# Kernel tuning notes

Measured on AMD Instinct MI355X. Metric: run time of the kernel, lower is better.

## Reference

```python
import jax, jax.numpy as jnp
import numpy as np

N_NODES = 100000
N_EDGES = 3200000
IN_SIZE = 256
HID_SIZE = 256
OUT_SIZE = 64


def setup_inputs() -> dict:
    key = jax.random.key(0)
    ks = jax.random.split(key, 8)
    X = jax.random.normal(ks[0], (N_NODES, IN_SIZE), dtype=jnp.float32)
    edge_vals = jax.random.uniform(ks[1], (N_EDGES,), dtype=jnp.float32)
    # xavier-uniform-ish init for weights
    lim1 = float(np.sqrt(6.0 / (IN_SIZE + HID_SIZE)))
    W1 = jax.random.uniform(ks[2], (IN_SIZE, HID_SIZE), minval=-lim1, maxval=lim1, dtype=jnp.float32)
    b1 = jnp.zeros((HID_SIZE,), dtype=jnp.float32)
    lim2 = float(np.sqrt(6.0 / (HID_SIZE + OUT_SIZE)))
    W2 = jax.random.uniform(ks[3], (HID_SIZE, OUT_SIZE), minval=-lim2, maxval=lim2, dtype=jnp.float32)
    b2 = jnp.zeros((OUT_SIZE,), dtype=jnp.float32)
    row = jnp.sort(jax.random.randint(ks[4], (N_EDGES,), 0, N_NODES, dtype=jnp.int32))
    col = jax.random.randint(ks[5], (N_EDGES,), 0, N_NODES, dtype=jnp.int32)
    return {"X": X, "edge_vals": edge_vals, "W1": W1, "b1": b1,
            "W2": W2, "b2": b2, "row": row, "col": col}


def reference(X, edge_vals, W1, b1, W2, b2, row, col):
    """2-layer GCN (eval mode, dropout = identity).

    A is a sparse NxN matrix in COO form: A[row[e], col[e]] = edge_vals[e].
    Layer: relu(A @ (X @ W1) + b1); output: A @ (h @ W2) + b2.
    """
    n = X.shape[0]

    def spmm(dense):  # (A @ dense): gather columns, scale, segment-sum over rows
        gathered = edge_vals[:, None] * dense[col]        # [E, F]
        return jax.ops.segment_sum(gathered, row, num_segments=n)

    h = spmm(X @ W1) + b1          # [N, HID]
    h = jax.nn.relu(h)
    out = spmm(h @ W2) + b2        # [N, OUT]
    return out
```

## Files before the change

### kernel.cpp

```cpp
#include <hip/hip_runtime.h>


constexpr int IN_SIZE = 256;
constexpr int HID = 256;
constexpr int OUTF = 64;

typedef __bf16 bf16x8 __attribute__((ext_vector_type(8)));
typedef float f32x4 __attribute__((ext_vector_type(4)));

__device__ __forceinline__ ushort f2b(float f) {
    uint u = __float_as_uint(f);
    uint r = (u + 0x7fffu + ((u >> 16) & 1u)) >> 16;
    return (ushort)r;
}
__device__ __forceinline__ float b2f(ushort h) {
    return __uint_as_float(((uint)h) << 16);
}

__global__ void setup_kernel(const int* __restrict__ row, int* __restrict__ rp,
                             const float* __restrict__ W1, ushort* __restrict__ W1T,
                             const float* __restrict__ W2, ushort* __restrict__ W2T,
                             int n, int E, int rpB) {
    int b = blockIdx.x;
    if (b < rpB) {
        int i = b * 256 + threadIdx.x;
        if (i > n) return;
        int lo = 0, hi = E;
        while (lo < hi) {
            int mid = (lo + hi) >> 1;
            if (row[mid] < i) lo = mid + 1; else hi = mid;
        }
        rp[i] = lo;
    } else if (b < rpB + 256) {
        int nn = b - rpB;
        int k = threadIdx.x;
        W1T[(size_t)nn * 256 + k] = f2b(W1[(size_t)k * 256 + nn]);
    } else {
        int nn = b - rpB - 256;
        int k = threadIdx.x;
        W2T[(size_t)nn * 256 + k] = f2b(W2[(size_t)k * 64 + nn]);
    }
}

__global__ void prep_edges(const float* __restrict__ vals, const int* __restrict__ col,
                           const float* __restrict__ s, int2* __restrict__ ew,
                           int E, int shift) {
    int e = blockIdx.x * 256 + threadIdx.x;
    if (e >= E) return;
    int c = col[e];
    ew[e] = make_int2(c << shift, __float_as_int(vals[e] * s[c]));
}

__global__ __launch_bounds__(512)
void gemm1_q(const float* __restrict__ A, const ushort* __restrict__ Bt,
             char* __restrict__ Q, float* __restrict__ s1, int M) {
    constexpr int K = 256;
    __shared__ ushort As[128 * 40];
    __shared__ ushort Bs[256 * 40];
    __shared__ float red[4][128];
    __shared__ float fin[128];
    const int tid = threadIdx.x;
    const int wave = tid >> 6, lane = tid & 63;
    const int quad = lane >> 4, l = lane & 15;
    const int wr = wave >> 2, wc = wave & 3;
    const int m0 = blockIdx.x * 128;

    const int ar = tid >> 2;
    const int ak = (tid & 3) * 8;
    const size_t aoff = (size_t)min(m0 + ar, M - 1) * K + ak;
    const int bn = tid >> 2;
    const int bkp = (tid & 3) * 8;

    f32x4 acc[4][4] = {};

    for (int k0 = 0; k0 < K; k0 += 32) {
        float4 a0 = *(const float4*)(A + aoff + k0);
        float4 a1 = *(const float4*)(A + aoff + k0 + 4);
        uint4 bv0 = *(const uint4*)(Bt + (size_t)bn * K + k0 + bkp);
        uint4 bv1 = *(const uint4*)(Bt + (size_t)(bn + 128) * K + k0 + bkp);
        uint4 pa;
        pa.x = (uint)f2b(a0.x) | ((uint)f2b(a0.y) << 16);
        pa.y = (uint)f2b(a0.z) | ((uint)f2b(a0.w) << 16);
        pa.z = (uint)f2b(a1.x) | ((uint)f2b(a1.y) << 16);
        pa.w = (uint)f2b(a1.z) | ((uint)f2b(a1.w) << 16);
        __syncthreads();
        *(uint4*)&As[ar * 40 + ak] = pa;
        *(uint4*)&Bs[bn * 40 + bkp] = bv0;
        *(uint4*)&Bs[(bn + 128) * 40 + bkp] = bv1;
        __syncthreads();

        bf16x8 af[4], bfr[4];
#pragma unroll
        for (int mt = 0; mt < 4; ++mt)
            af[mt] = *(const bf16x8*)&As[(wr * 64 + mt * 16 + l) * 40 + quad * 8];
#pragma unroll
        for (int nt = 0; nt < 4; ++nt)
            bfr[nt] = *(const bf16x8*)&Bs[(wc * 64 + nt * 16 + l) * 40 + quad * 8];
#pragma unroll
        for (int mt = 0; mt < 4; ++mt)
#pragma unroll
            for (int nt = 0; nt < 4; ++nt)
                acc[mt][nt] = __builtin_amdgcn_mfma_f32_16x16x32_bf16(
                    af[mt], bfr[nt], acc[mt][nt], 0, 0, 0);
    }

    float rmax[4][4];
#pragma unroll
    for (int mt = 0; mt < 4; ++mt)
#pragma unroll
        for (int reg = 0; reg < 4; ++reg) {
            float m = 0.f;
#pragma unroll
            for (int nt = 0; nt < 4; ++nt)
                m = fmaxf(m, fabsf(acc[mt][nt][reg]));
            rmax[mt][reg] = m;
        }
#pragma unroll
    for (int s = 1; s <= 8; s <<= 1)
#pragma unroll
        for (int mt = 0; mt < 4; ++mt)
#pragma unroll
            for (int reg = 0; reg < 4; ++reg)
                rmax[mt][reg] = fmaxf(rmax[mt][reg], __shfl_xor(rmax[mt][reg], s));
    if (l < 4) {
#pragma unroll
        for (int mt = 0; mt < 4; ++mt)
            red[wc][wr * 64 + mt * 16 + quad * 4 + l] = rmax[mt][l];
    }
    __syncthreads();
    if (tid < 128) {
        float m = fmaxf(fmaxf(red[0][tid], red[1][tid]),
                        fmaxf(red[2][tid], red[3][tid]));
        fin[tid] = m;
        int r = m0 + tid;
        if (r < M) s1[r] = m * (1.f / 127.f);
    }
    __syncthreads();

#pragma unroll
    for (int mt = 0; mt < 4; ++mt)
#pragma unroll
        for (int reg = 0; reg < 4; ++reg) {
            int rl = wr * 64 + mt * 16 + quad * 4 + reg;
            int r = m0 + rl;
            if (r >= M) continue;
            float m = fin[rl];
            float inv = m > 0.f ? 127.f / m : 0.f;
#pragma unroll
            for (int nt = 0; nt < 4; ++nt) {
                int c = wc * 64 + nt * 16 + l;
                Q[(size_t)r * 256 + c] = (char)(int)rintf(acc[mt][nt][reg] * inv);
            }
        }
}

__global__ __launch_bounds__(256, 4)
void gemm2_q(const ushort* __restrict__ A, const ushort* __restrict__ Bt,
             char* __restrict__ Q, float* __restrict__ s2, int M) {
    constexpr int K = 256;
    __shared__ ushort As[128 * 40];
    __shared__ ushort Bs[64 * 40];
    __shared__ float red[2][128];
    __shared__ float fin[128];
    const int tid = threadIdx.x;
    const int wave = tid >> 6, lane = tid & 63;
    const int quad = lane >> 4, l = lane & 15;
    const int wr = wave >> 1, wc = wave & 1;
    const int m0 = blockIdx.x * 128;

    const int crow = tid >> 2;
    const int cpart = (tid & 3) * 8;
    const size_t aoff0 = (size_t)min(m0 + crow, M - 1) * K + cpart;
    const size_t aoff1 = (size_t)min(m0 + crow + 64, M - 1) * K + cpart;
    const size_t boff  = (size_t)crow * K + cpart;

    f32x4 acc[4][2] = {};

    for (int k0 = 0; k0 < K; k0 += 32) {
        uint4 a0 = *(const uint4*)(A + aoff0 + k0);
        uint4 a1 = *(const uint4*)(A + aoff1 + k0);
        uint4 b0 = *(const uint4*)(Bt + boff + k0);
        __syncthreads();
        *(uint4*)&As[crow * 40 + cpart] = a0;
        *(uint4*)&As[(crow + 64) * 40 + cpart] = a1;
        *(uint4*)&Bs[crow * 40 + cpart] = b0;
        __syncthreads();

        bf16x8 af[4], bfr[2];
        const ushort* ab = &As[(wr * 64 + l) * 40 + quad * 8];
#pragma unroll
        for (int mt = 0; mt < 4; ++mt)
            af[mt] = *(const bf16x8*)(ab + mt * 16 * 40);
        const ushort* bb = &Bs[(wc * 32 + l) * 40 + quad * 8];
#pragma unroll
        for (int nt = 0; nt < 2; ++nt)
            bfr[nt] = *(const bf16x8*)(bb + nt * 16 * 40);
#pragma unroll
        for (int mt = 0; mt < 4; ++mt)
#pragma unroll
            for (int nt = 0; nt < 2; ++nt)
                acc[mt][nt] = __builtin_amdgcn_mfma_f32_16x16x32_bf16(
                    af[mt], bfr[nt], acc[mt][nt], 0, 0, 0);
    }

    float rmax[4][4];
#pragma unroll
    for (int mt = 0; mt < 4; ++mt)
#pragma unroll
        for (int reg = 0; reg < 4; ++reg)
            rmax[mt][reg] = fmaxf(fabsf(acc[mt][0][reg]), fabsf(acc[mt][1][reg]));
#pragma unroll
    for (int s = 1; s <= 8; s <<= 1)
#pragma unroll
        for (int mt = 0; mt < 4; ++mt)
#pragma unroll
            for (int reg = 0; reg < 4; ++reg)
                rmax[mt][reg] = fmaxf(rmax[mt][reg], __shfl_xor(rmax[mt][reg], s));
    if (l < 4) {
#pragma unroll
        for (int mt = 0; mt < 4; ++mt)
            red[wc][wr * 64 + mt * 16 + quad * 4 + l] = rmax[mt][l];
    }
    __syncthreads();
    if (tid < 128) {
        float m = fmaxf(red[0][tid], red[1][tid]);
        fin[tid] = m;
        int r = m0 + tid;
        if (r < M) s2[r] = m * (1.f / 127.f);
    }
    __syncthreads();

#pragma unroll
    for (int mt = 0; mt < 4; ++mt)
#pragma unroll
        for (int reg = 0; reg < 4; ++reg) {
            int rl = wr * 64 + mt * 16 + quad * 4 + reg;
            int r = m0 + rl;
            if (r >= M) continue;
            float m = fin[rl];
            float inv = m > 0.f ? 127.f / m : 0.f;
#pragma unroll
            for (int nt = 0; nt < 2; ++nt) {
                int c = wc * 32 + nt * 16 + l;
                Q[(size_t)r * 64 + c] = (char)(int)rintf(acc[mt][nt][reg] * inv);
            }
        }
}

__global__ __launch_bounds__(256)
void spmm1_q(const char* __restrict__ Q, const int2* __restrict__ ew,
             const int* __restrict__ rp, const float* __restrict__ bias,
             ushort* __restrict__ H, int n) {
    const int wave = threadIdx.x >> 6;
    const int lane = threadIdx.x & 63;
    const int node = blockIdx.x * 4 + wave;
    if (node >= n) return;
    const int e0 = rp[node], e1 = rp[node + 1];
    float a0 = 0.f, a1 = 0.f, a2 = 0.f, a3 = 0.f;
    int e = e0;
    for (; e + 7 < e1; e += 8) {
#pragma unroll
        for (int u = 0; u < 8; ++u) {
            int2 m = ew[e + u];
            float w = __int_as_float(m.y);
            char4 q = *(const char4*)(Q + (size_t)(uint)m.x + lane * 4);
            a0 += w * (float)q.x;
            a1 += w * (float)q.y;
            a2 += w * (float)q.z;
            a3 += w * (float)q.w;
        }
    }
    for (; e < e1; ++e) {
        int2 m = ew[e];
        float w = __int_as_float(m.y);
        char4 q = *(const char4*)(Q + (size_t)(uint)m.x + lane * 4);
        a0 += w * (float)q.x;
        a1 += w * (float)q.y;
        a2 += w * (float)q.z;
        a3 += w * (float)q.w;
    }
    float4 b = *(const float4*)(bias + lane * 4);
    ushort4 r;
    r.x = f2b(fmaxf(a0 + b.x, 0.f));
    r.y = f2b(fmaxf(a1 + b.y, 0.f));
    r.z = f2b(fmaxf(a2 + b.z, 0.f));
    r.w = f2b(fmaxf(a3 + b.w, 0.f));
    *(ushort4*)(H + (size_t)node * 256 + lane * 4) = r;
}

__global__ __launch_bounds__(256)
void spmm2_q(const char* __restrict__ Q, const int2* __restrict__ ew,
             const int* __restrict__ rp, const float* __restrict__ bias,
             float* __restrict__ O, int n) {
    const int wave = threadIdx.x >> 6;
    const int lane = threadIdx.x & 63;
    const int node = blockIdx.x * 4 + wave;
    if (node >= n) return;
    const int e0 = rp[node], e1 = rp[node + 1];
    float acc = 0.f;
    int e = e0;
    for (; e + 15 < e1; e += 16) {
#pragma unroll
        for (int u = 0; u < 16; ++u) {
            int2 m = ew[e + u];
            acc += __int_as_float(m.y) * (float)Q[(size_t)(uint)m.x + lane];
        }
    }
    for (; e + 3 < e1; e += 4) {
#pragma unroll
        for (int u = 0; u < 4; ++u) {
            int2 m = ew[e + u];
            acc += __int_as_float(m.y) * (float)Q[(size_t)(uint)m.x + lane];
        }
    }
    for (; e < e1; ++e) {
        int2 m = ew[e];
        acc += __int_as_float(m.y) * (float)Q[(size_t)(uint)m.x + lane];
    }
    O[(size_t)node * 64 + lane] = acc + bias[lane];
}

static inline size_t alignup(size_t x) { return (x + 255) & ~(size_t)255; }

extern "C" void kernel_launch(void* const* d_in, const int* in_sizes, int n_in,
                              void* d_out, int out_size, void* d_ws, size_t ws_size,
                              hipStream_t stream) {
    const float* X  = (const float*)d_in[0];
    const float* ev = (const float*)d_in[1];
    const float* W1 = (const float*)d_in[2];
    const float* b1 = (const float*)d_in[3];
    const float* W2 = (const float*)d_in[4];
    const float* b2 = (const float*)d_in[5];
    const int*  row = (const int*)d_in[6];
    const int*  col = (const int*)d_in[7];
    float* out = (float*)d_out;

    const int n = in_sizes[0] / IN_SIZE;
    const int E = in_sizes[1];

    char* p = (char*)d_ws;
    ushort* H    = (ushort*)p; p += alignup((size_t)n * HID * 2);
    char*   Q1   = (char*)p;   p += alignup((size_t)n * HID);
    float*  s1   = (float*)p;  p += alignup((size_t)n * 4);
    char*   Q2   = (char*)p;   p += alignup((size_t)n * OUTF);
    float*  s2   = (float*)p;  p += alignup((size_t)n * 4);
    ushort* W1T  = (ushort*)p; p += alignup((size_t)IN_SIZE * HID * 2);
    ushort* W2T  = (ushort*)p; p += alignup((size_t)HID * OUTF * 2);
    int*    rp   = (int*)p;    p += alignup((size_t)(n + 1) * 4);
    int2*   ewb  = (int2*)p;   p += alignup((size_t)E * 8);

    const int rpB = (n + 1 + 255) / 256;
    setup_kernel<<<rpB + 256 + 64, 256, 0, stream>>>(row, rp, W1, W1T, W2, W2T,
                                                     n, E, rpB);

    gemm1_q<<<(n + 127) / 128, 512, 0, stream>>>(X, W1T, Q1, s1, n);

    prep_edges<<<(E + 255) / 256, 256, 0, stream>>>(ev, col, s1, ewb, E, 8);

    spmm1_q<<<(n + 3) / 4, 256, 0, stream>>>(Q1, ewb, rp, b1, H, n);

    gemm2_q<<<(n + 127) / 128, 256, 0, stream>>>(H, W2T, Q2, s2, n);

    prep_edges<<<(E + 255) / 256, 256, 0, stream>>>(ev, col, s2, ewb, E, 6);

    spmm2_q<<<(n + 3) / 4, 256, 0, stream>>>(Q2, ewb, rp, b2, out, n);
}
```

Baseline: 472.9 us.

## Fuse edge-weight prep into SpMM kernels and register-prefetch GEMM tiles

Removes the two prep_edges passes that materialised packed (col, val*scale) pairs. Each SpMM now reads col and vals directly with aligned vector loads, after a scalar head loop that brings the edge index to a multiple of four. It gathers the per-node scale s[c] inline and batches 16 gathers before accumulating. This saves two extra kernel launches and the write and reread of an 8-byte-per-edge buffer, at the cost of an extra random gather of s per edge. Both GEMMs also prefetch the next K-slice from global memory into registers before doing the current slice's MFMA work, to overlap load latency.

Measured after the change: 496.9 us. +5.1%, slower.

```diff
diff --git a/kernel.cpp b/kernel.cpp
--- a/kernel.cpp
+++ b/kernel.cpp
@@ -12,9 +12,6 @@
     uint u = __float_as_uint(f);
     uint r = (u + 0x7fffu + ((u >> 16) & 1u)) >> 16;
     return (ushort)r;
-}
-__device__ __forceinline__ float b2f(ushort h) {
-    return __uint_as_float(((uint)h) << 16);
 }
 
 __global__ void setup_kernel(const int* __restrict__ row, int* __restrict__ rp,
@@ -40,15 +37,6 @@
         int k = threadIdx.x;
         W2T[(size_t)nn * 256 + k] = f2b(W2[(size_t)k * 64 + nn]);
     }
-}
-
-__global__ void prep_edges(const float* __restrict__ vals, const int* __restrict__ col,
-                           const float* __restrict__ s, int2* __restrict__ ew,
-                           int E, int shift) {
-    int e = blockIdx.x * 256 + threadIdx.x;
-    if (e >= E) return;
-    int c = col[e];
-    ew[e] = make_int2(c << shift, __float_as_int(vals[e] * s[c]));
 }
 
 __global__ __launch_bounds__(512)
@@ -70,14 +58,17 @@
     const size_t aoff = (size_t)min(m0 + ar, M - 1) * K + ak;
     const int bn = tid >> 2;
     const int bkp = (tid & 3) * 8;
+    const size_t boff0 = (size_t)bn * K + bkp;
+    const size_t boff1 = (size_t)(bn + 128) * K + bkp;
 
     f32x4 acc[4][4] = {};
 
+    float4 a0 = *(const float4*)(A + aoff);
+    float4 a1 = *(const float4*)(A + aoff + 4);
+    uint4 bv0 = *(const uint4*)(Bt + boff0);
+    uint4 bv1 = *(const uint4*)(Bt + boff1);
+
     for (int k0 = 0; k0 < K; k0 += 32) {
-        float4 a0 = *(const float4*)(A + aoff + k0);
-        float4 a1 = *(const float4*)(A + aoff + k0 + 4);
-        uint4 bv0 = *(const uint4*)(Bt + (size_t)bn * K + k0 + bkp);
-        uint4 bv1 = *(const uint4*)(Bt + (size_t)(bn + 128) * K + k0 + bkp);
         uint4 pa;
         pa.x = (uint)f2b(a0.x) | ((uint)f2b(a0.y) << 16);
         pa.y = (uint)f2b(a0.z) | ((uint)f2b(a0.w) << 16);
@@ -88,6 +79,13 @@
         *(uint4*)&Bs[bn * 40 + bkp] = bv0;
         *(uint4*)&Bs[(bn + 128) * 40 + bkp] = bv1;
         __syncthreads();
+
+        if (k0 + 32 < K) {
+            a0 = *(const float4*)(A + aoff + k0 + 32);
+            a1 = *(const float4*)(A + aoff + k0 + 36);
+            bv0 = *(const uint4*)(Bt + boff0 + k0 + 32);
+            bv1 = *(const uint4*)(Bt + boff1 + k0 + 32);
+        }
 
         bf16x8 af[4], bfr[4];
 #pragma unroll
@@ -176,15 +174,22 @@
 
     f32x4 acc[4][2] = {};
 
+    uint4 a0 = *(const uint4*)(A + aoff0);
+    uint4 a1 = *(const uint4*)(A + aoff1);
+    uint4 b0 = *(const uint4*)(Bt + boff);
+
     for (int k0 = 0; k0 < K; k0 += 32) {
-        uint4 a0 = *(const uint4*)(A + aoff0 + k0);
-        uint4 a1 = *(const uint4*)(A + aoff1 + k0);
-        uint4 b0 = *(const uint4*)(Bt + boff + k0);
         __syncthreads();
         *(uint4*)&As[crow * 40 + cpart] = a0;
         *(uint4*)&As[(crow + 64) * 40 + cpart] = a1;
         *(uint4*)&Bs[crow * 40 + cpart] = b0;
         __syncthreads();
+
+        if (k0 + 32 < K) {
+            a0 = *(const uint4*)(A + aoff0 + k0 + 32);
+            a1 = *(const uint4*)(A + aoff1 + k0 + 32);
+            b0 = *(const uint4*)(Bt + boff + k0 + 32);
+        }
 
         bf16x8 af[4], bfr[2];
         const ushort* ab = &As[(wr * 64 + l) * 40 + quad * 8];
@@ -248,7 +253,8 @@
 }
 
 __global__ __launch_bounds__(256)
-void spmm1_q(const char* __restrict__ Q, const int2* __restrict__ ew,
+void spmm1_q(const char* __restrict__ Q, const int* __restrict__ col,
+             const float* __restrict__ vals, const float* __restrict__ s,
              const int* __restrict__ rp, const float* __restrict__ bias,
              ushort* __restrict__ H, int n) {
     const int wave = threadIdx.x >> 6;
@@ -256,40 +262,90 @@
     const int node = blockIdx.x * 4 + wave;
     if (node >= n) return;
     const int e0 = rp[node], e1 = rp[node + 1];
+    const int lb = lane * 4;
     float a0 = 0.f, a1 = 0.f, a2 = 0.f, a3 = 0.f;
     int e = e0;
-    for (; e + 7 < e1; e += 8) {
-#pragma unroll
-        for (int u = 0; u < 8; ++u) {
-            int2 m = ew[e + u];
-            float w = __int_as_float(m.y);
-            char4 q = *(const char4*)(Q + (size_t)(uint)m.x + lane * 4);
-            a0 += w * (float)q.x;
-            a1 += w * (float)q.y;
-            a2 += w * (float)q.z;
-            a3 += w * (float)q.w;
-        }
-    }
-    for (; e < e1; ++e) {
-        int2 m = ew[e];
-        float w = __int_as_float(m.y);
-        char4 q = *(const char4*)(Q + (size_t)(uint)m.x + lane * 4);
+    int ehead = min(e1, (e0 + 3) & ~3);
+    for (; e < ehead; ++e) {
+        int c = col[e];
+        float w = vals[e] * s[c];
+        char4 q = *(const char4*)(Q + ((size_t)(uint)c << 8) + lb);
         a0 += w * (float)q.x;
         a1 += w * (float)q.y;
         a2 += w * (float)q.z;
         a3 += w * (float)q.w;
     }
-    float4 b = *(const float4*)(bias + lane * 4);
+    for (; e + 15 < e1; e += 16) {
+        int4 c0 = *(const int4*)(col + e);
+        int4 c1 = *(const int4*)(col + e + 4);
+        int4 c2 = *(const int4*)(col + e + 8);
+        int4 c3 = *(const int4*)(col + e + 12);
+        float4 v0 = *(const float4*)(vals + e);
+        float4 v1 = *(const float4*)(vals + e + 4);
+        float4 v2 = *(const float4*)(vals + e + 8);
+        float4 v3 = *(const float4*)(vals + e + 12);
+        const int cc[16] = {c0.x, c0.y, c0.z, c0.w, c1.x, c1.y, c1.z, c1.w,
+                            c2.x, c2.y, c2.z, c2.w, c3.x, c3.y, c3.z, c3.w};
+        const float vv[16] = {v0.x, v0.y, v0.z, v0.w, v1.x, v1.y, v1.z, v1.w,
+                              v2.x, v2.y, v2.z, v2.w, v3.x, v3.y, v3.z, v3.w};
+        char4 q[16];
+        float w[16];
+#pragma unroll
+        for (int u = 0; u < 16; ++u)
+            q[u] = *(const char4*)(Q + ((size_t)(uint)cc[u] << 8) + lb);
+#pragma unroll
+        for (int u = 0; u < 16; ++u)
+            w[u] = vv[u] * s[cc[u]];
+#pragma unroll
+        for (int u = 0; u < 16; ++u) {
+            a0 += w[u] * (float)q[u].x;
+            a1 += w[u] * (float)q[u].y;
+            a2 += w[u] * (float)q[u].z;
+            a3 += w[u] * (float)q[u].w;
+        }
+    }
+    for (; e + 3 < e1; e += 4) {
+        int4 c0 = *(const int4*)(col + e);
+        float4 v0 = *(const float4*)(vals + e);
+        const int cc[4] = {c0.x, c0.y, c0.z, c0.w};
+        const float vv[4] = {v0.x, v0.y, v0.z, v0.w};
+        char4 q[4];
+        float w[4];
+#pragma unroll
+        for (int u = 0; u < 4; ++u)
+            q[u] = *(const char4*)(Q + ((size_t)(uint)cc[u] << 8) + lb);
+#pragma unroll
+        for (int u = 0; u < 4; ++u)
+            w[u] = vv[u] * s[cc[u]];
+#pragma unroll
+        for (int u = 0; u < 4; ++u) {
+            a0 += w[u] * (float)q[u].x;
+            a1 += w[u] * (float)q[u].y;
+            a2 += w[u] * (float)q[u].z;
+            a3 += w[u] * (float)q[u].w;
+        }
+    }
+    for (; e < e1; ++e) {
+        int c = col[e];
+        float w = vals[e] * s[c];
+        char4 q = *(const char4*)(Q + ((size_t)(uint)c << 8) + lb);
+        a0 += w * (float)q.x;
+        a1 += w * (float)q.y;
+        a2 += w * (float)q.z;
+        a3 += w * (float)q.w;
+    }
+    float4 b = *(const float4*)(bias + lb);
     ushort4 r;
     r.x = f2b(fmaxf(a0 + b.x, 0.f));
     r.y = f2b(fmaxf(a1 + b.y, 0.f));
     r.z = f2b(fmaxf(a2 + b.z, 0.f));
     r.w = f2b(fmaxf(a3 + b.w, 0.f));
-    *(ushort4*)(H + (size_t)node * 256 + lane * 4) = r;
+    *(ushort4*)(H + (size_t)node * 256 + lb) = r;
 }
 
 __global__ __launch_bounds__(256)
-void spmm2_q(const char* __restrict__ Q, const int2* __restrict__ ew,
+void spmm2_q(const char* __restrict__ Q, const int* __restrict__ col,
+             const float* __restrict__ vals, const float* __restrict__ s,
              const int* __restrict__ rp, const float* __restrict__ bias,
              float* __restrict__ O, int n) {
     const int wave = threadIdx.x >> 6;
@@ -299,23 +355,58 @@
     const int e0 = rp[node], e1 = rp[node + 1];
     float acc = 0.f;
     int e = e0;
+    int ehead = min(e1, (e0 + 3) & ~3);
+    for (; e < ehead; ++e) {
+        int c = col[e];
+        float w = vals[e] * s[c];
+        acc += w * (float)Q[((size_t)(uint)c << 6) + lane];
+    }
     for (; e + 15 < e1; e += 16) {
-#pragma unroll
-        for (int u = 0; u < 16; ++u) {
-            int2 m = ew[e + u];
-            acc += __int_as_float(m.y) * (float)Q[(size_t)(uint)m.x + lane];
-        }
+        int4 c0 = *(const int4*)(col + e);
+        int4 c1 = *(const int4*)(col + e + 4);
+        int4 c2 = *(const int4*)(col + e + 8);
+        int4 c3 = *(const int4*)(col + e + 12);
+        float4 v0 = *(const float4*)(vals + e);
+        float4 v1 = *(const float4*)(vals + e + 4);
+        float4 v2 = *(const float4*)(vals + e + 8);
+        float4 v3 = *(const float4*)(vals + e + 12);
+        const int cc[16] = {c0.x, c0.y, c0.z, c0.w, c1.x, c1.y, c1.z, c1.w,
+                            c2.x, c2.y, c2.z, c2.w, c3.x, c3.y, c3.z, c3.w};
+        const float vv[16] = {v0.x, v0.y, v0.z, v0.w, v1.x, v1.y, v1.z, v1.w,
+                              v2.x, v2.y, v2.z, v2.w, v3.x, v3.y, v3.z, v3.w};
+        char qb[16];
+        float w[16];
+#pragma unroll
+        for (int u = 0; u < 16; ++u)
+            qb[u] = Q[((size_t)(uint)cc[u] << 6) + lane];
+#pragma unroll
+        for (int u = 0; u < 16; ++u)
+            w[u] = vv[u] * s[cc[u]];
+#pragma unroll
+        for (int u = 0; u < 16; ++u)
+            acc += w[u] * (float)qb[u];
     }
     for (; e + 3 < e1; e += 4) {
-#pragma unroll
-        for (int u = 0; u < 4; ++u) {
-            int2 m = ew[e + u];
-            acc += __int_as_float(m.y) * (float)Q[(size_t)(uint)m.x + lane];
-        }
+        int4 c0 = *(const int4*)(col + e);
+        float4 v0 = *(const float4*)(vals + e);
+        const int cc[4] = {c0.x, c0.y, c0.z, c0.w};
+        const float vv[4] = {v0.x, v0.y, v0.z, v0.w};
+        char qb[4];
+        float w[4];
+#pragma unroll
+        for (int u = 0; u < 4; ++u)
+            qb[u] = Q[((size_t)(uint)cc[u] << 6) + lane];
+#pragma unroll
+        for (int u = 0; u < 4; ++u)
+            w[u] = vv[u] * s[cc[u]];
+#pragma unroll
+        for (int u = 0; u < 4; ++u)
+            acc += w[u] * (float)qb[u];
     }
     for (; e < e1; ++e) {
-        int2 m = ew[e];
-        acc += __int_as_float(m.y) * (float)Q[(size_t)(uint)m.x + lane];
+        int c = col[e];
+        float w = vals[e] * s[c];
+        acc += w * (float)Q[((size_t)(uint)c << 6) + lane];
     }
     O[(size_t)node * 64 + lane] = acc + bias[lane];
 }
@@ -347,7 +438,6 @@
     ushort* W1T  = (ushort*)p; p += alignup((size_t)IN_SIZE * HID * 2);
     ushort* W2T  = (ushort*)p; p += alignup((size_t)HID * OUTF * 2);
     int*    rp   = (int*)p;    p += alignup((size_t)(n + 1) * 4);
-    int2*   ewb  = (int2*)p;   p += alignup((size_t)E * 8);
 
     const int rpB = (n + 1 + 255) / 256;
     setup_kernel<<<rpB + 256 + 64, 256, 0, stream>>>(row, rp, W1, W1T, W2, W2T,
@@ -355,13 +445,9 @@
 
     gemm1_q<<<(n + 127) / 128, 512, 0, stream>>>(X, W1T, Q1, s1, n);
 
-    prep_edges<<<(E + 255) / 256, 256, 0, stream>>>(ev, col, s1, ewb, E, 8);
-
-    spmm1_q<<<(n + 3) / 4, 256, 0, stream>>>(Q1, ewb, rp, b1, H, n);
+    spmm1_q<<<(n + 3) / 4, 256, 0, stream>>>(Q1, col, ev, s1, rp, b1, H, n);
 
     gemm2_q<<<(n + 127) / 128, 256, 0, stream>>>(H, W2T, Q2, s2, n);
 
-    prep_edges<<<(E + 255) / 256, 256, 0, stream>>>(ev, col, s2, ewb, E, 6);
-
-    spmm2_q<<<(n + 3) / 4, 256, 0, stream>>>(Q2, ewb, rp, b2, out, n);
-}
+    spmm2_q<<<(n + 3) / 4, 256, 0, stream>>>(Q2, col, ev, s2, rp, b2, out, n);
+}
```

## Widen SpMM gathers with edge-parallel lane groups and offset-uint8 quantization

Applied to the files above, without the earlier changes.

The SpMM kernels now split each wave into lane groups that process different edges at once, with each lane loading 16 (or 8) bytes of quantized features per gather instead of 4 (or 1). Partial sums are then combined with cross-lane shuffles. Quantized values are stored as unsigned bytes offset by 128, so conversion uses cheap shifts and masks, and the offset is removed using the summed edge weights. Both GEMMs also register-prefetch the next K tile while the current one is computed. This trades more registers and shuffle work for fewer, wider memory transactions and more loads in flight.

New measurement: 454.8 us. 1.04x faster.

```diff
diff --git a/kernel.cpp b/kernel.cpp
--- a/kernel.cpp
+++ b/kernel.cpp
@@ -13,8 +13,12 @@
     uint r = (u + 0x7fffu + ((u >> 16) & 1u)) >> 16;
     return (ushort)r;
 }
-__device__ __forceinline__ float b2f(ushort h) {
-    return __uint_as_float(((uint)h) << 16);
+
+__device__ __forceinline__ void fma4(float* a, uint word, float w) {
+    a[0] += w * (float)(word & 0xffu);
+    a[1] += w * (float)((word >> 8) & 0xffu);
+    a[2] += w * (float)((word >> 16) & 0xffu);
+    a[3] += w * (float)(word >> 24);
 }
 
 __global__ void setup_kernel(const int* __restrict__ row, int* __restrict__ rp,
@@ -53,7 +57,7 @@
 
 __global__ __launch_bounds__(512)
 void gemm1_q(const float* __restrict__ A, const ushort* __restrict__ Bt,
-             char* __restrict__ Q, float* __restrict__ s1, int M) {
+             unsigned char* __restrict__ Q, float* __restrict__ s1, int M) {
     constexpr int K = 256;
     __shared__ ushort As[128 * 40];
     __shared__ ushort Bs[256 * 40];
@@ -70,14 +74,17 @@
     const size_t aoff = (size_t)min(m0 + ar, M - 1) * K + ak;
     const int bn = tid >> 2;
     const int bkp = (tid & 3) * 8;
+    const size_t boff0 = (size_t)bn * K + bkp;
+    const size_t boff1 = (size_t)(bn + 128) * K + bkp;
 
     f32x4 acc[4][4] = {};
 
+    float4 a0 = *(const float4*)(A + aoff);
+    float4 a1 = *(const float4*)(A + aoff + 4);
+    uint4 bv0 = *(const uint4*)(Bt + boff0);
+    uint4 bv1 = *(const uint4*)(Bt + boff1);
+
     for (int k0 = 0; k0 < K; k0 += 32) {
-        float4 a0 = *(const float4*)(A + aoff + k0);
-        float4 a1 = *(const float4*)(A + aoff + k0 + 4);
-        uint4 bv0 = *(const uint4*)(Bt + (size_t)bn * K + k0 + bkp);
-        uint4 bv1 = *(const uint4*)(Bt + (size_t)(bn + 128) * K + k0 + bkp);
         uint4 pa;
         pa.x = (uint)f2b(a0.x) | ((uint)f2b(a0.y) << 16);
         pa.y = (uint)f2b(a0.z) | ((uint)f2b(a0.w) << 16);
@@ -89,6 +96,13 @@
         *(uint4*)&Bs[(bn + 128) * 40 + bkp] = bv1;
         __syncthreads();
 
+        if (k0 + 32 < K) {
+            a0 = *(const float4*)(A + aoff + k0 + 32);
+            a1 = *(const float4*)(A + aoff + k0 + 36);
+            bv0 = *(const uint4*)(Bt + boff0 + k0 + 32);
+            bv1 = *(const uint4*)(Bt + boff1 + k0 + 32);
+        }
+
         bf16x8 af[4], bfr[4];
 #pragma unroll
         for (int mt = 0; mt < 4; ++mt)
@@ -149,14 +163,15 @@
 #pragma unroll
             for (int nt = 0; nt < 4; ++nt) {
                 int c = wc * 64 + nt * 16 + l;
-                Q[(size_t)r * 256 + c] = (char)(int)rintf(acc[mt][nt][reg] * inv);
+                Q[(size_t)r * 256 + c] =
+                    (unsigned char)((int)rintf(acc[mt][nt][reg] * inv) + 128);
             }
         }
 }
 
 __global__ __launch_bounds__(256, 4)
 void gemm2_q(const ushort* __restrict__ A, const ushort* __restrict__ Bt,
-             char* __restrict__ Q, float* __restrict__ s2, int M) {
+             unsigned char* __restrict__ Q, float* __restrict__ s2, int M) {
     constexpr int K = 256;
     __shared__ ushort As[128 * 40];
     __shared__ ushort Bs[64 * 40];
@@ -176,15 +191,22 @@
 
     f32x4 acc[4][2] = {};
 
+    uint4 a0 = *(const uint4*)(A + aoff0);
+    uint4 a1 = *(const uint4*)(A + aoff1);
+    uint4 b0 = *(const uint4*)(Bt + boff);
+
     for (int k0 = 0; k0 < K; k0 += 32) {
-        uint4 a0 = *(const uint4*)(A + aoff0 + k0);
-        uint4 a1 = *(const uint4*)(A + aoff1 + k0);
-        uint4 b0 = *(const uint4*)(Bt + boff + k0);
         __syncthreads();
         *(uint4*)&As[crow * 40 + cpart] = a0;
         *(uint4*)&As[(crow + 64) * 40 + cpart] = a1;
         *(uint4*)&Bs[crow * 40 + cpart] = b0;
         __syncthreads();
+
+        if (k0 + 32 < K) {
+            a0 = *(const uint4*)(A + aoff0 + k0 + 32);
+            a1 = *(const uint4*)(A + aoff1 + k0 + 32);
+            b0 = *(const uint4*)(Bt + boff + k0 + 32);
+        }
 
         bf16x8 af[4], bfr[2];
         const ushort* ab = &As[(wr * 64 + l) * 40 + quad * 8];
@@ -242,13 +264,14 @@
 #pragma unroll
             for (int nt = 0; nt < 2; ++nt) {
                 int c = wc * 32 + nt * 16 + l;
-                Q[(size_t)r * 64 + c] = (char)(int)rintf(acc[mt][nt][reg] * inv);
+                Q[(size_t)r * 64 + c] =
+                    (unsigned char)((int)rintf(acc[mt][nt][reg] * inv) + 128);
             }
         }
 }
 
 __global__ __launch_bounds__(256)
-void spmm1_q(const char* __restrict__ Q, const int2* __restrict__ ew,
+void spmm1_q(const unsigned char* __restrict__ Q, const int2* __restrict__ ew,
              const int* __restrict__ rp, const float* __restrict__ bias,
              ushort* __restrict__ H, int n) {
     const int wave = threadIdx.x >> 6;
@@ -256,40 +279,76 @@
     const int node = blockIdx.x * 4 + wave;
     if (node >= n) return;
     const int e0 = rp[node], e1 = rp[node + 1];
-    float a0 = 0.f, a1 = 0.f, a2 = 0.f, a3 = 0.f;
+    const int g = lane >> 4;
+    const int fb = (lane & 15) * 16;
+
+    float acc[16] = {};
+    float sumw = 0.f;
     int e = e0;
-    for (; e + 7 < e1; e += 8) {
-#pragma unroll
-        for (int u = 0; u < 8; ++u) {
-            int2 m = ew[e + u];
+    for (; e + 16 <= e1; e += 16) {
+#pragma unroll
+        for (int u = 0; u < 4; ++u) {
+            int2 m = ew[e + u * 4 + g];
             float w = __int_as_float(m.y);
-            char4 q = *(const char4*)(Q + (size_t)(uint)m.x + lane * 4);
-            a0 += w * (float)q.x;
-            a1 += w * (float)q.y;
-            a2 += w * (float)q.z;
-            a3 += w * (float)q.w;
-        }
-    }
-    for (; e < e1; ++e) {
-        int2 m = ew[e];
-        float w = __int_as_float(m.y);
-        char4 q = *(const char4*)(Q + (size_t)(uint)m.x + lane * 4);
-        a0 += w * (float)q.x;
-        a1 += w * (float)q.y;
-        a2 += w * (float)q.z;
-        a3 += w * (float)q.w;
-    }
-    float4 b = *(const float4*)(bias + lane * 4);
-    ushort4 r;
-    r.x = f2b(fmaxf(a0 + b.x, 0.f));
-    r.y = f2b(fmaxf(a1 + b.y, 0.f));
-    r.z = f2b(fmaxf(a2 + b.z, 0.f));
-    r.w = f2b(fmaxf(a3 + b.w, 0.f));
-    *(ushort4*)(H + (size_t)node * 256 + lane * 4) = r;
+            uint4 qv = *(const uint4*)(Q + (size_t)(uint)m.x + fb);
+            sumw += w;
+            fma4(&acc[0], qv.x, w);
+            fma4(&acc[4], qv.y, w);
+            fma4(&acc[8], qv.z, w);
+            fma4(&acc[12], qv.w, w);
+        }
+    }
+    for (; e < e1; e += 4) {
+        int idx = e + g;
+        int2 m = ew[idx];
+        bool ok = idx < e1;
+        uint off = ok ? (uint)m.x : 0u;
+        float w = ok ? __int_as_float(m.y) : 0.f;
+        uint4 qv = *(const uint4*)(Q + (size_t)off + fb);
+        sumw += w;
+        fma4(&acc[0], qv.x, w);
+        fma4(&acc[4], qv.y, w);
+        fma4(&acc[8], qv.z, w);
+        fma4(&acc[12], qv.w, w);
+    }
+
+#pragma unroll
+    for (int s = 16; s <= 32; s <<= 1) {
+#pragma unroll
+        for (int j = 0; j < 16; ++j)
+            acc[j] += __shfl_xor(acc[j], s);
+        sumw += __shfl_xor(sumw, s);
+    }
+
+    if (g == 0) {
+        const int f0 = (lane & 15) * 16;
+        float4 b0 = *(const float4*)(bias + f0);
+        float4 b1 = *(const float4*)(bias + f0 + 4);
+        float4 b2 = *(const float4*)(bias + f0 + 8);
+        float4 b3 = *(const float4*)(bias + f0 + 12);
+        float bb[16] = {b0.x, b0.y, b0.z, b0.w, b1.x, b1.y, b1.z, b1.w,
+                        b2.x, b2.y, b2.z, b2.w, b3.x, b3.y, b3.z, b3.w};
+        float fix = -128.f * sumw;
+        ushort r[16];
+#pragma unroll
+        for (int j = 0; j < 16; ++j)
+            r[j] = f2b(fmaxf(acc[j] + fix + bb[j], 0.f));
+        uint4 w0, w1;
+        w0.x = (uint)r[0] | ((uint)r[1] << 16);
+        w0.y = (uint)r[2] | ((uint)r[3] << 16);
+        w0.z = (uint)r[4] | ((uint)r[5] << 16);
+        w0.w = (uint)r[6] | ((uint)r[7] << 16);
+        w1.x = (uint)r[8] | ((uint)r[9] << 16);
+        w1.y = (uint)r[10] | ((uint)r[11] << 16);
+        w1.z = (uint)r[12] | ((uint)r[13] << 16);
+        w1.w = (uint)r[14] | ((uint)r[15] << 16);
+        *(uint4*)(H + (size_t)node * 256 + f0) = w0;
+        *(uint4*)(H + (size_t)node * 256 + f0 + 8) = w1;
+    }
 }
 
 __global__ __launch_bounds__(256)
-void spmm2_q(const char* __restrict__ Q, const int2* __restrict__ ew,
+void spmm2_q(const unsigned char* __restrict__ Q, const int2* __restrict__ ew,
              const int* __restrict__ rp, const float* __restrict__ bias,
              float* __restrict__ O, int n) {
     const int wave = threadIdx.x >> 6;
@@ -297,27 +356,60 @@
     const int node = blockIdx.x * 4 + wave;
     if (node >= n) return;
     const int e0 = rp[node], e1 = rp[node + 1];
-    float acc = 0.f;
+    const int g = lane >> 3;
+    const int fb = (lane & 7) * 8;
+
+    float acc[8] = {};
+    float sumw = 0.f;
     int e = e0;
-    for (; e + 15 < e1; e += 16) {
-#pragma unroll
-        for (int u = 0; u < 16; ++u) {
-            int2 m = ew[e + u];
-            acc += __int_as_float(m.y) * (float)Q[(size_t)(uint)m.x + lane];
-        }
-    }
-    for (; e + 3 < e1; e += 4) {
-#pragma unroll
-        for (int u = 0; u < 4; ++u) {
-            int2 m = ew[e + u];
-            acc += __int_as_float(m.y) * (float)Q[(size_t)(uint)m.x + lane];
-        }
-    }
-    for (; e < e1; ++e) {
-        int2 m = ew[e];
-        acc += __int_as_float(m.y) * (float)Q[(size_t)(uint)m.x + lane];
-    }
-    O[(size_t)node * 64 + lane] = acc + bias[lane];
+    for (; e + 16 <= e1; e += 16) {
+#pragma unroll
+        for (int u = 0; u < 2; ++u) {
+            int2 m = ew[e + u * 8 + g];
+            float w = __int_as_float(m.y);
+            uint2 qv = *(const uint2*)(Q + (size_t)(uint)m.x + fb);
+            sumw += w;
+            fma4(&acc[0], qv.x, w);
+            fma4(&acc[4], qv.y, w);
+        }
+    }
+    for (; e < e1; e += 8) {
+        int idx = e + g;
+        int2 m = ew[idx];
+        bool ok = idx < e1;
+        uint off = ok ? (uint)m.x : 0u;
+        float w = ok ? __int_as_float(m.y) : 0.f;
+        uint2 qv = *(const uint2*)(Q + (size_t)off + fb);
+        sumw += w;
+        fma4(&acc[0], qv.x, w);
+        fma4(&acc[4], qv.y, w);
+    }
+
+#pragma unroll
+    for (int s = 8; s <= 32; s <<= 1) {
+#pragma unroll
+        for (int j = 0; j < 8; ++j)
+            acc[j] += __shfl_xor(acc[j], s);
+        sumw += __shfl_xor(sumw, s);
+    }
+
+    if (g == 0) {
+        const int f0 = (lane & 7) * 8;
+        float4 b0 = *(const float4*)(bias + f0);
+        float4 b1 = *(const float4*)(bias + f0 + 4);
+        float fix = -128.f * sumw;
+        float4 o0, o1;
+        o0.x = acc[0] + fix + b0.x;
+        o0.y = acc[1] + fix + b0.y;
+        o0.z = acc[2] + fix + b0.z;
+        o0.w = acc[3] + fix + b0.w;
+        o1.x = acc[4] + fix + b1.x;
+        o1.y = acc[5] + fix + b1.y;
+        o1.z = acc[6] + fix + b1.z;
+        o1.w = acc[7] + fix + b1.w;
+        *(float4*)(O + (size_t)node * 64 + f0) = o0;
+        *(float4*)(O + (size_t)node * 64 + f0 + 4) = o1;
+    }
 }
 
 static inline size_t alignup(size_t x) { return (x + 255) & ~(size_t)255; }
@@ -340,14 +432,14 @@
 
     char* p = (char*)d_ws;
     ushort* H    = (ushort*)p; p += alignup((size_t)n * HID * 2);
-    char*   Q1   = (char*)p;   p += alignup((size_t)n * HID);
+    unsigned char* Q1 = (unsigned char*)p; p += alignup((size_t)n * HID);
     float*  s1   = (float*)p;  p += alignup((size_t)n * 4);
-    char*   Q2   = (char*)p;   p += alignup((size_t)n * OUTF);
+    unsigned char* Q2 = (unsigned char*)p; p += alignup((size_t)n * OUTF);
     float*  s2   = (float*)p;  p += alignup((size_t)n * 4);
     ushort* W1T  = (ushort*)p; p += alignup((size_t)IN_SIZE * HID * 2);
     ushort* W2T  = (ushort*)p; p += alignup((size_t)HID * OUTF * 2);
     int*    rp   = (int*)p;    p += alignup((size_t)(n + 1) * 4);
-    int2*   ewb  = (int2*)p;   p += alignup((size_t)E * 8);
+    int2*   ewb  = (int2*)p;   p += alignup((size_t)(E + 16) * 8);
 
     const int rpB = (n + 1 + 255) / 256;
     setup_kernel<<<rpB + 256 + 64, 256, 0, stream>>>(row, rp, W1, W1T, W2, W2T,
```

## Slice quantized features by 32 columns and pack edge weight+index into one word

Applied to the files above, without the earlier changes.

The GEMMs now write int8 outputs biased to uint8 in a column-sliced layout (32-feature slices), and edges are packed into a single 32-bit word holding a truncated 15-bit-mantissa weight and a 17-bit column index. The SpMM kernels are restructured so each block handles one feature slice, with half-waves processing a node and 8 edge groups in parallel, followed by a shuffle reduction and a -128*sum(w) correction. The GEMM loops also gain register prefetch of the next K tile. Intended to halve edge metadata traffic and improve gather locality per slice; risks reduced weight precision, a 17-bit node index limit (131072), and re-reading edge data once per slice.

After: 605.8 us. 28.1% more time.

```diff
diff --git a/kernel.cpp b/kernel.cpp
--- a/kernel.cpp
+++ b/kernel.cpp
@@ -7,14 +7,12 @@
 
 typedef __bf16 bf16x8 __attribute__((ext_vector_type(8)));
 typedef float f32x4 __attribute__((ext_vector_type(4)));
+typedef uint u32x4 __attribute__((ext_vector_type(4)));
 
 __device__ __forceinline__ ushort f2b(float f) {
     uint u = __float_as_uint(f);
     uint r = (u + 0x7fffu + ((u >> 16) & 1u)) >> 16;
     return (ushort)r;
-}
-__device__ __forceinline__ float b2f(ushort h) {
-    return __uint_as_float(((uint)h) << 16);
 }
 
 __global__ void setup_kernel(const int* __restrict__ row, int* __restrict__ rp,
@@ -42,18 +40,19 @@
     }
 }
 
-__global__ void prep_edges(const float* __restrict__ vals, const int* __restrict__ col,
-                           const float* __restrict__ s, int2* __restrict__ ew,
-                           int E, int shift) {
+__global__ void prep_pack(const float* __restrict__ vals, const int* __restrict__ col,
+                          const float* __restrict__ s, uint* __restrict__ ewc, int E) {
     int e = blockIdx.x * 256 + threadIdx.x;
     if (e >= E) return;
     int c = col[e];
-    ew[e] = make_int2(c << shift, __float_as_int(vals[e] * s[c]));
+    float w = vals[e] * s[c];
+    uint wb = (__float_as_uint(w) + 0x10000u) & 0xFFFE0000u;
+    ewc[e] = wb | (uint)c;
 }
 
 __global__ __launch_bounds__(512)
 void gemm1_q(const float* __restrict__ A, const ushort* __restrict__ Bt,
-             char* __restrict__ Q, float* __restrict__ s1, int M) {
+             unsigned char* __restrict__ Q, float* __restrict__ s1, int M) {
     constexpr int K = 256;
     __shared__ ushort As[128 * 40];
     __shared__ ushort Bs[256 * 40];
@@ -64,20 +63,24 @@
     const int quad = lane >> 4, l = lane & 15;
     const int wr = wave >> 2, wc = wave & 3;
     const int m0 = blockIdx.x * 128;
+    const size_t sstr = (size_t)M * 32;
 
     const int ar = tid >> 2;
     const int ak = (tid & 3) * 8;
     const size_t aoff = (size_t)min(m0 + ar, M - 1) * K + ak;
     const int bn = tid >> 2;
     const int bkp = (tid & 3) * 8;
+    const size_t boff0 = (size_t)bn * K + bkp;
+    const size_t boff1 = (size_t)(bn + 128) * K + bkp;
 
     f32x4 acc[4][4] = {};
 
+    float4 a0 = *(const float4*)(A + aoff);
+    float4 a1 = *(const float4*)(A + aoff + 4);
+    uint4 bv0 = *(const uint4*)(Bt + boff0);
+    uint4 bv1 = *(const uint4*)(Bt + boff1);
+
     for (int k0 = 0; k0 < K; k0 += 32) {
-        float4 a0 = *(const float4*)(A + aoff + k0);
-        float4 a1 = *(const float4*)(A + aoff + k0 + 4);
-        uint4 bv0 = *(const uint4*)(Bt + (size_t)bn * K + k0 + bkp);
-        uint4 bv1 = *(const uint4*)(Bt + (size_t)(bn + 128) * K + k0 + bkp);
         uint4 pa;
         pa.x = (uint)f2b(a0.x) | ((uint)f2b(a0.y) << 16);
         pa.y = (uint)f2b(a0.z) | ((uint)f2b(a0.w) << 16);
@@ -89,6 +92,13 @@
         *(uint4*)&Bs[(bn + 128) * 40 + bkp] = bv1;
         __syncthreads();
 
+        if (k0 + 32 < K) {
+            a0 = *(const float4*)(A + aoff + k0 + 32);
+            a1 = *(const float4*)(A + aoff + k0 + 36);
+            bv0 = *(const uint4*)(Bt + boff0 + k0 + 32);
+            bv1 = *(const uint4*)(Bt + boff1 + k0 + 32);
+        }
+
         bf16x8 af[4], bfr[4];
 #pragma unroll
         for (int mt = 0; mt < 4; ++mt)
@@ -149,14 +159,15 @@
 #pragma unroll
             for (int nt = 0; nt < 4; ++nt) {
                 int c = wc * 64 + nt * 16 + l;
-                Q[(size_t)r * 256 + c] = (char)(int)rintf(acc[mt][nt][reg] * inv);
+                Q[(size_t)(c >> 5) * sstr + (size_t)r * 32 + (c & 31)] =
+                    (unsigned char)((int)rintf(acc[mt][nt][reg] * inv) + 128);
             }
         }
 }
 
 __global__ __launch_bounds__(256, 4)
 void gemm2_q(const ushort* __restrict__ A, const ushort* __restrict__ Bt,
-             char* __restrict__ Q, float* __restrict__ s2, int M) {
+             unsigned char* __restrict__ Q, float* __restrict__ s2, int M) {
     constexpr int K = 256;
     __shared__ ushort As[128 * 40];
     __shared__ ushort Bs[64 * 40];
@@ -167,6 +178,7 @@
     const int quad = lane >> 4, l = lane & 15;
     const int wr = wave >> 1, wc = wave & 1;
     const int m0 = blockIdx.x * 128;
+    const size_t sstr = (size_t)M * 32;
 
     const int crow = tid >> 2;
     const int cpart = (tid & 3) * 8;
@@ -176,15 +188,22 @@
 
     f32x4 acc[4][2] = {};
 
+    uint4 a0 = *(const uint4*)(A + aoff0);
+    uint4 a1 = *(const uint4*)(A + aoff1);
+    uint4 b0 = *(const uint4*)(Bt + boff);
+
     for (int k0 = 0; k0 < K; k0 += 32) {
-        uint4 a0 = *(const uint4*)(A + aoff0 + k0);
-        uint4 a1 = *(const uint4*)(A + aoff1 + k0);
-        uint4 b0 = *(const uint4*)(Bt + boff + k0);
         __syncthreads();
         *(uint4*)&As[crow * 40 + cpart] = a0;
         *(uint4*)&As[(crow + 64) * 40 + cpart] = a1;
         *(uint4*)&Bs[crow * 40 + cpart] = b0;
         __syncthreads();
+
+        if (k0 + 32 < K) {
+            a0 = *(const uint4*)(A + aoff0 + k0 + 32);
+            a1 = *(const uint4*)(A + aoff1 + k0 + 32);
+            b0 = *(const uint4*)(Bt + boff + k0 + 32);
+        }
 
         bf16x8 af[4], bfr[2];
         const ushort* ab = &As[(wr * 64 + l) * 40 + quad * 8];
@@ -242,82 +261,151 @@
 #pragma unroll
             for (int nt = 0; nt < 2; ++nt) {
                 int c = wc * 32 + nt * 16 + l;
-                Q[(size_t)r * 64 + c] = (char)(int)rintf(acc[mt][nt][reg] * inv);
+                Q[(size_t)(c >> 5) * sstr + (size_t)r * 32 + (c & 31)] =
+                    (unsigned char)((int)rintf(acc[mt][nt][reg] * inv) + 128);
             }
         }
 }
 
 __global__ __launch_bounds__(256)
-void spmm1_q(const char* __restrict__ Q, const int2* __restrict__ ew,
+void spmm1_s(const unsigned char* __restrict__ Q, const uint* __restrict__ ewc,
              const int* __restrict__ rp, const float* __restrict__ bias,
              ushort* __restrict__ H, int n) {
+    const int slice = blockIdx.x & 7;
+    const int nb = blockIdx.x >> 3;
     const int wave = threadIdx.x >> 6;
     const int lane = threadIdx.x & 63;
-    const int node = blockIdx.x * 4 + wave;
-    if (node >= n) return;
-    const int e0 = rp[node], e1 = rp[node + 1];
-    float a0 = 0.f, a1 = 0.f, a2 = 0.f, a3 = 0.f;
-    int e = e0;
-    for (; e + 7 < e1; e += 8) {
-#pragma unroll
-        for (int u = 0; u < 8; ++u) {
-            int2 m = ew[e + u];
-            float w = __int_as_float(m.y);
-            char4 q = *(const char4*)(Q + (size_t)(uint)m.x + lane * 4);
-            a0 += w * (float)q.x;
-            a1 += w * (float)q.y;
-            a2 += w * (float)q.z;
-            a3 += w * (float)q.w;
-        }
-    }
-    for (; e < e1; ++e) {
-        int2 m = ew[e];
-        float w = __int_as_float(m.y);
-        char4 q = *(const char4*)(Q + (size_t)(uint)m.x + lane * 4);
-        a0 += w * (float)q.x;
-        a1 += w * (float)q.y;
-        a2 += w * (float)q.z;
-        a3 += w * (float)q.w;
-    }
-    float4 b = *(const float4*)(bias + lane * 4);
-    ushort4 r;
-    r.x = f2b(fmaxf(a0 + b.x, 0.f));
-    r.y = f2b(fmaxf(a1 + b.y, 0.f));
-    r.z = f2b(fmaxf(a2 + b.z, 0.f));
-    r.w = f2b(fmaxf(a3 + b.w, 0.f));
-    *(ushort4*)(H + (size_t)node * 256 + lane * 4) = r;
+    const int hl = lane & 31;
+    const int g = hl >> 2;
+    const int fl = lane & 3;
+    const int fb = fl * 8;
+    const int node = nb * 8 + wave * 2 + (lane >> 5);
+    const unsigned char* Qs = Q + (size_t)slice * ((size_t)n << 5);
+
+    int e0 = 0, e1 = 0;
+    if (node < n) { e0 = rp[node]; e1 = rp[node + 1]; }
+    int deg = e1 - e0;
+    int dmax = max(deg, __shfl_xor(deg, 32));
+
+    float acc[8] = {};
+    float sumw = 0.f;
+    int eh = e0 + g;
+    for (int it = (dmax + 15) >> 4; it > 0; --it, eh += 16) {
+        bool ok0 = eh < e1;
+        bool ok1 = eh + 8 < e1;
+        uint p0 = __builtin_nontemporal_load(ewc + (ok0 ? eh : 0));
+        uint p1 = __builtin_nontemporal_load(ewc + (ok1 ? eh + 8 : 0));
+        float w0 = ok0 ? __uint_as_float(p0 & 0xFFFE0000u) : 0.f;
+        float w1 = ok1 ? __uint_as_float(p1 & 0xFFFE0000u) : 0.f;
+        uint of0 = (ok0 ? ((p0 & 0x1FFFFu) << 5) : 0u) + fb;
+        uint of1 = (ok1 ? ((p1 & 0x1FFFFu) << 5) : 0u) + fb;
+        uint2 q0 = *(const uint2*)(Qs + of0);
+        uint2 q1 = *(const uint2*)(Qs + of1);
+        sumw += w0 + w1;
+        acc[0] += w0 * (float)(q0.x & 0xffu)         + w1 * (float)(q1.x & 0xffu);
+        acc[1] += w0 * (float)((q0.x >> 8) & 0xffu)  + w1 * (float)((q1.x >> 8) & 0xffu);
+        acc[2] += w0 * (float)((q0.x >> 16) & 0xffu) + w1 * (float)((q1.x >> 16) & 0xffu);
+        acc[3] += w0 * (float)(q0.x >> 24)           + w1 * (float)(q1.x >> 24);
+        acc[4] += w0 * (float)(q0.y & 0xffu)         + w1 * (float)(q1.y & 0xffu);
+        acc[5] += w0 * (float)((q0.y >> 8) & 0xffu)  + w1 * (float)((q1.y >> 8) & 0xffu);
+        acc[6] += w0 * (float)((q0.y >> 16) & 0xffu) + w1 * (float)((q1.y >> 16) & 0xffu);
+        acc[7] += w0 * (float)(q0.y >> 24)           + w1 * (float)(q1.y >> 24);
+    }
+
+#pragma unroll
+    for (int s = 4; s <= 16; s <<= 1) {
+#pragma unroll
+        for (int j = 0; j < 8; ++j)
+            acc[j] += __shfl_xor(acc[j], s);
+        sumw += __shfl_xor(sumw, s);
+    }
+
+    if (g == 0 && node < n) {
+        const float* bp = bias + slice * 32 + fb;
+        float fix = -128.f * sumw;
+        ushort r[8];
+#pragma unroll
+        for (int j = 0; j < 8; ++j)
+            r[j] = f2b(fmaxf(acc[j] + fix + bp[j], 0.f));
+        u32x4 wv;
+        wv.x = (uint)r[0] | ((uint)r[1] << 16);
+        wv.y = (uint)r[2] | ((uint)r[3] << 16);
+        wv.z = (uint)r[4] | ((uint)r[5] << 16);
+        wv.w = (uint)r[6] | ((uint)r[7] << 16);
+        __builtin_nontemporal_store(wv,
+            (u32x4*)(H + (size_t)node * 256 + slice * 32 + fb));
+    }
 }
 
 __global__ __launch_bounds__(256)
-void spmm2_q(const char* __restrict__ Q, const int2* __restrict__ ew,
+void spmm2_s(const unsigned char* __restrict__ Q, const uint* __restrict__ ewc,
              const int* __restrict__ rp, const float* __restrict__ bias,
              float* __restrict__ O, int n) {
+    const int slice = blockIdx.x & 1;
+    const int nb = blockIdx.x >> 1;
     const int wave = threadIdx.x >> 6;
     const int lane = threadIdx.x & 63;
-    const int node = blockIdx.x * 4 + wave;
-    if (node >= n) return;
-    const int e0 = rp[node], e1 = rp[node + 1];
-    float acc = 0.f;
-    int e = e0;
-    for (; e + 15 < e1; e += 16) {
-#pragma unroll
-        for (int u = 0; u < 16; ++u) {
-            int2 m = ew[e + u];
-            acc += __int_as_float(m.y) * (float)Q[(size_t)(uint)m.x + lane];
-        }
-    }
-    for (; e + 3 < e1; e += 4) {
-#pragma unroll
-        for (int u = 0; u < 4; ++u) {
-            int2 m = ew[e + u];
-            acc += __int_as_float(m.y) * (float)Q[(size_t)(uint)m.x + lane];
-        }
-    }
-    for (; e < e1; ++e) {
-        int2 m = ew[e];
-        acc += __int_as_float(m.y) * (float)Q[(size_t)(uint)m.x + lane];
-    }
-    O[(size_t)node * 64 + lane] = acc + bias[lane];
+    const int hl = lane & 31;
+    const int g = hl >> 2;
+    const int fl = lane & 3;
+    const int fb = fl * 8;
+    const int node = nb * 8 + wave * 2 + (lane >> 5);
+    const unsigned char* Qs = Q + (size_t)slice * ((size_t)n << 5);
+
+    int e0 = 0, e1 = 0;
+    if (node < n) { e0 = rp[node]; e1 = rp[node + 1]; }
+    int deg = e1 - e0;
+    int dmax = max(deg, __shfl_xor(deg, 32));
+
+    float acc[8] = {};
+    float sumw = 0.f;
+    int eh = e0 + g;
+    for (int it = (dmax + 15) >> 4; it > 0; --it, eh += 16) {
+        bool ok0 = eh < e1;
+        bool ok1 = eh + 8 < e1;
+        uint p0 = __builtin_nontemporal_load(ewc + (ok0 ? eh : 0));
+        uint p1 = __builtin_nontemporal_load(ewc + (ok1 ? eh + 8 : 0));
+        float w0 = ok0 ? __uint_as_float(p0 & 0xFFFE0000u) : 0.f;
+        float w1 = ok1 ? __uint_as_float(p1 & 0xFFFE0000u) : 0.f;
+        uint of0 = (ok0 ? ((p0 & 0x1FFFFu) << 5) : 0u) + fb;
+        uint of1 = (ok1 ? ((p1 & 0x1FFFFu) << 5) : 0u) + fb;
+        uint2 q0 = *(const uint2*)(Qs + of0);
+        uint2 q1 = *(const uint2*)(Qs + of1);
+        sumw += w0 + w1;
+        acc[0] += w0 * (float)(q0.x & 0xffu)         + w1 * (float)(q1.x & 0xffu);
+        acc[1] += w0 * (float)((q0.x >> 8) & 0xffu)  + w1 * (float)((q1.x >> 8) & 0xffu);
+        acc[2] += w0 * (float)((q0.x >> 16) & 0xffu) + w1 * (float)((q1.x >> 16) & 0xffu);
+        acc[3] += w0 * (float)(q0.x >> 24)           + w1 * (float)(q1.x >> 24);
+        acc[4] += w0 * (float)(q0.y & 0xffu)         + w1 * (float)(q1.y & 0xffu);
+        acc[5] += w0 * (float)((q0.y >> 8) & 0xffu)  + w1 * (float)((q1.y >> 8) & 0xffu);
+        acc[6] += w0 * (float)((q0.y >> 16) & 0xffu) + w1 * (float)((q1.y >> 16) & 0xffu);
+        acc[7] += w0 * (float)(q0.y >> 24)           + w1 * (float)(q1.y >> 24);
+    }
+
+#pragma unroll
+    for (int s = 4; s <= 16; s <<= 1) {
+#pragma unroll
+        for (int j = 0; j < 8; ++j)
+            acc[j] += __shfl_xor(acc[j], s);
+        sumw += __shfl_xor(sumw, s);
+    }
+
+    if (g == 0 && node < n) {
+        const float* bp = bias + slice * 32 + fb;
+        float fix = -128.f * sumw;
+        f32x4 o0, o1;
+        o0.x = acc[0] + fix + bp[0];
+        o0.y = acc[1] + fix + bp[1];
+        o0.z = acc[2] + fix + bp[2];
+        o0.w = acc[3] + fix + bp[3];
+        o1.x = acc[4] + fix + bp[4];
+        o1.y = acc[5] + fix + bp[5];
+        o1.z = acc[6] + fix + bp[6];
+        o1.w = acc[7] + fix + bp[7];
+        float* op = O + (size_t)node * 64 + slice * 32 + fb;
+        __builtin_nontemporal_store(o0, (f32x4*)op);
+        __builtin_nontemporal_store(o1, (f32x4*)(op + 4));
+    }
 }
 
 static inline size_t alignup(size_t x) { return (x + 255) & ~(size_t)255; }
@@ -340,14 +428,14 @@
 
     char* p = (char*)d_ws;
     ushort* H    = (ushort*)p; p += alignup((size_t)n * HID * 2);
-    char*   Q1   = (char*)p;   p += alignup((size_t)n * HID);
+    unsigned char* Q1 = (unsigned char*)p; p += alignup((size_t)n * HID);
     float*  s1   = (float*)p;  p += alignup((size_t)n * 4);
-    char*   Q2   = (char*)p;   p += alignup((size_t)n * OUTF);
+    unsigned char* Q2 = (unsigned char*)p; p += alignup((size_t)n * OUTF);
     float*  s2   = (float*)p;  p += alignup((size_t)n * 4);
     ushort* W1T  = (ushort*)p; p += alignup((size_t)IN_SIZE * HID * 2);
     ushort* W2T  = (ushort*)p; p += alignup((size_t)HID * OUTF * 2);
     int*    rp   = (int*)p;    p += alignup((size_t)(n + 1) * 4);
-    int2*   ewb  = (int2*)p;   p += alignup((size_t)E * 8);
+    uint*   ewc  = (uint*)p;   p += alignup((size_t)E * 4);
 
     const int rpB = (n + 1 + 255) / 256;
     setup_kernel<<<rpB + 256 + 64, 256, 0, stream>>>(row, rp, W1, W1T, W2, W2T,
@@ -355,13 +443,14 @@
 
     gemm1_q<<<(n + 127) / 128, 512, 0, stream>>>(X, W1T, Q1, s1, n);
 
-    prep_edges<<<(E + 255) / 256, 256, 0, stream>>>(ev, col, s1, ewb, E, 8);
-
-    spmm1_q<<<(n + 3) / 4, 256, 0, stream>>>(Q1, ewb, rp, b1, H, n);
+    prep_pack<<<(E + 255) / 256, 256, 0, stream>>>(ev, col, s1, ewc, E);
+
+    const int nb1 = (n + 7) / 8;
+    spmm1_s<<<nb1 * 8, 256, 0, stream>>>(Q1, ewc, rp, b1, H, n);
 
     gemm2_q<<<(n + 127) / 128, 256, 0, stream>>>(H, W2T, Q2, s2, n);
 
-    prep_edges<<<(E + 255) / 256, 256, 0, stream>>>(ev, col, s2, ewb, E, 6);
-
-    spmm2_q<<<(n + 3) / 4, 256, 0, stream>>>(Q2, ewb, rp, b2, out, n);
-}
+    prep_pack<<<(E + 255) / 256, 256, 0, stream>>>(ev, col, s2, ewc, E);
+
+    spmm2_s<<<nb1 * 2, 256, 0, stream>>>(Q2, ewc, rp, b2, out, n);
+}
```
